# Kernel tuning notes

Measured on AMD Instinct MI355X. Metric: run time of the kernel, lower is better.

The kernel has to match this reference:

```python
import jax, jax.numpy as jnp
from jax import lax
import numpy as np

EPS = 1e-12      # F.normalize eps
TOP_N = 250      # top negatives selected
SMOOTH = 1e-5    # soft dice smooth


def _dilate10(m):
    # == 10 iterations of 3x3x3 binary max-pool dilation. m: [B,D,H,W] float.
    for _ in range(10):
        m = lax.reduce_window(m, 0.0, lax.max, (1, 3, 3, 3), (1, 1, 1, 1), 'SAME')
    return m


def _self_loss(feature, lab):
    # feature: [B,C,D,H,W], lab: [B,D,H,W] int
    feat = jnp.moveaxis(feature, 1, -1)                       # [B,D,H,W,C]
    pos = (lab == 1)
    posf = pos.astype(feat.dtype)
    cnt = posf.sum()
    std = (feat * posf[..., None]).sum((0, 1, 2, 3)) / jnp.maximum(cnt, 1.0)
    std = jnp.where(cnt > 0, std, 0.0)                        # [C]
    std_n = std / jnp.maximum(jnp.linalg.norm(std), EPS)
    feat_n = feat / jnp.maximum(jnp.linalg.norm(feat, axis=-1, keepdims=True), EPS)
    # cosine similarity of per-voxel normalized features vs normalized mean positive
    sim = jnp.einsum('bdhwc,c->bdhw', feat_n, std_n)

    # positive term: mean over positives of (1 - sim)
    pos_loss = jnp.where(cnt > 0, ((1.0 - sim) * posf).sum() / jnp.maximum(cnt, 1.0), 0.0)

    # easily-misclassified ring: dilate(pos,10) & ~pos; mean relu(sim)
    mis = (_dilate10(posf) > 0) & (~pos)
    misf = mis.astype(sim.dtype)
    mcnt = misf.sum()
    mis_loss = jnp.where(mcnt > 0, (jax.nn.relu(sim) * misf).sum() / jnp.maximum(mcnt, 1.0), 0.0)

    # hard negatives: top-250 sims among label==0, scatter to mask, dilate, & ~pos
    neg = (lab == 0)
    neg_sims = jnp.where(neg, sim, -jnp.inf).reshape(-1)
    top_vals, top_idx = lax.top_k(neg_sims, TOP_N)
    hsm = jnp.zeros(neg_sims.shape[0], sim.dtype).at[top_idx].set(
        jnp.where(jnp.isfinite(top_vals), 1.0, 0.0)).reshape(sim.shape)
    fin = (_dilate10(hsm) > 0) & (~pos)
    finf = fin.astype(sim.dtype)
    fcnt = finf.sum()
    neg_loss = jnp.where(fcnt > 0, (jax.nn.relu(sim) * finf).sum() / jnp.maximum(fcnt, 1.0), 0.0)

    return pos_loss + mis_loss + neg_loss


def _ce_dice(net_output, target):
    lab = target[:, 0]                                        # [B,D,H,W]
    logp = jax.nn.log_softmax(net_output, axis=1)
    ce = -jnp.mean(jnp.take_along_axis(logp, target, axis=1))
    probs = jnp.exp(logp)                                     # softmax_helper_dim1
    nc = net_output.shape[1]
    onehot = jax.nn.one_hot(lab, nc, axis=1, dtype=probs.dtype)  # [B,nc,D,H,W]
    axes = (0, 2, 3, 4)                                       # batch_dice=True
    tp = (probs * onehot).sum(axes)
    fp = (probs * (1.0 - onehot)).sum(axes)
    fn = ((1.0 - probs) * onehot).sum(axes)
    dc = (2.0 * tp + SMOOTH) / (2.0 * tp + fp + fn + SMOOTH + 1e-8)
    dice = -jnp.mean(dc[1:])                                  # do_bg=False
    return ce, dice


def reference(feature, net_output, target):
    ce, dice = _ce_dice(net_output, target)
    sl = _self_loss(feature, target[:, 0])
    return 1.0 * ce + 1.0 * dice + 5.0 * sl


def setup_inputs():
    key = jax.random.key(0)
    k1, k2, k3 = jax.random.split(key, 3)
    B, C, D, H, W = 2, 32, 64, 128, 128
    NC = 2
    feature = jax.random.normal(k1, (B, C, D, H, W), jnp.float32)
    net_output = jax.random.normal(k2, (B, NC, D, H, W), jnp.float32)
    target = jax.random.randint(k3, (B, 1, D, H, W), 0, 2).astype(jnp.int32)
    return {'feature': feature, 'net_output': net_output, 'target': target}
```

## Files before the change

### kernel.cpp

```cpp
#include <hip/hip_runtime.h>
#include <stdint.h>

typedef unsigned int u32;
typedef unsigned long long u64;

#define BB 2
#define CC 32
#define DD 64
#define HH 128
#define WW 128
#define SS (DD*HH*WW)
#define NN (BB*SS)
#define NQ (NN/4)
#define NWORDS (NN/64)
#define EPSF 1e-12f
#define TOPN 250u

struct Ctrl {
  u32 done4, tie, pad0, pad1;
};

struct Acc {
  double ce, tp, fp, fn;
  double stdsum[CC];
  double pos_num, mis_num, fin_num;
  u64 cnt, mcnt, fcnt;
};

__device__ __forceinline__ float waveRedF(float v){
#pragma unroll
  for (int o = 32; o; o >>= 1) v += __shfl_xor(v, o);
  return v;
}
__device__ __forceinline__ u32 waveRedU(u32 v){
#pragma unroll
  for (int o = 32; o; o >>= 1) v += __shfl_xor(v, o);
  return v;
}
__device__ __forceinline__ void red_d(double* dst, float v, volatile float* sh){
  int lane = threadIdx.x & 63, wid = threadIdx.x >> 6;
  v = waveRedF(v);
  if (lane == 0) sh[wid] = v;
  __syncthreads();
  if (threadIdx.x == 0){
    float t = 0.f;
    for (int i = 0; i < (int)(blockDim.x >> 6); i++) t += sh[i];
    atomicAdd(dst, (double)t);
  }
  __syncthreads();
}
__device__ __forceinline__ void red_u(u64* dst, u32 v, volatile u32* sh){
  int lane = threadIdx.x & 63, wid = threadIdx.x >> 6;
  v = waveRedU(v);
  if (lane == 0) sh[wid] = v;
  __syncthreads();
  if (threadIdx.x == 0){
    u32 t = 0;
    for (int i = 0; i < (int)(blockDim.x >> 6); i++) t += sh[i];
    atomicAdd(dst, (u64)t);
  }
  __syncthreads();
}

__device__ __forceinline__ u32 sortkey(float f){
  u32 u = __float_as_uint(f);
  return (u & 0x80000000u) ? ~u : (u | 0x80000000u);
}

__device__ __forceinline__ void select_top(const u32* __restrict__ hist, u32 nbins,
                                           u32 k, u32* shres, u32* binOut, u32* kremOut){
  __syncthreads();
  if (threadIdx.x < 64){
    int lane = threadIdx.x;
    u32 running = 0; bool found = false;
    for (u32 chunk = 0; chunk * 64 < nbins && !found; chunk++){
      int bin = (int)nbins - 1 - (int)(chunk * 64 + (u32)lane);
      u32 val = (bin >= 0) ? hist[bin] : 0u;
      u32 p = val;
#pragma unroll
      for (int o = 1; o < 64; o <<= 1){ u32 t = __shfl_up(p, o); if (lane >= o) p += t; }
      u32 tot = __shfl(p, 63);
      u32 incl = running + p, excl = incl - val;
      bool hit = (excl < k) && (incl >= k);
      u64 mb = __ballot(hit);
      if (mb){
        int hl = __ffsll((unsigned long long)mb) - 1;
        if (lane == hl){ shres[0] = (u32)bin; shres[1] = k - excl; }
        found = true;
      } else running += tot;
    }
    if (!found && lane == 0){ shres[0] = 0; shres[1] = k; }
  }
  __syncthreads();
  *binOut = shres[0]; *kremOut = shres[1];
}

__global__ __launch_bounds__(256) void k_main1(const float* __restrict__ feat,
                                               const float* __restrict__ net,
                                               const int* __restrict__ tgt,
                                               u64* __restrict__ pbits, Acc* acc){
  __shared__ u32 nibsh[256];
  __shared__ float sacc[CC];
  __shared__ float shf[4]; __shared__ u32 shu[4];
  float a[CC];
#pragma unroll
  for (int c = 0; c < CC; c++) a[c] = 0.f;
  float ce = 0.f, tp = 0.f, fp = 0.f, fnn = 0.f;
  u32 cnt = 0;
  const u32 stride = 512u * 256u;
#pragma unroll 1
  for (u32 it = 0; it < 4; it++){
    u32 q = blockIdx.x * 256u + threadIdx.x + it * stride;
    u32 v = q * 4u;
    u32 b = v >> 20, s = v & (SS - 1);
    int4 l4 = *(const int4*)(tgt + v);
    u32 nib = (l4.x ? 1u : 0u) | (l4.y ? 2u : 0u) | (l4.z ? 4u : 0u) | (l4.w ? 8u : 0u);
    cnt += __popc(nib);
    __syncthreads();
    nibsh[threadIdx.x] = nib;
    {
      const float* nb = net + (size_t)(b * 2) * SS + s;
      float4 x0 = *(const float4*)(nb);
      float4 x1 = *(const float4*)(nb + SS);
      float xs0[4] = {x0.x, x0.y, x0.z, x0.w};
      float xs1[4] = {x1.x, x1.y, x1.z, x1.w};
#pragma unroll
      for (int j = 0; j < 4; j++){
        int lab = (nib >> j) & 1;
        float m = fmaxf(xs0[j], xs1[j]);
        float lse = m + logf(expf(xs0[j] - m) + expf(xs1[j] - m));
        ce += lse - (lab ? xs1[j] : xs0[j]);
        float p1 = expf(xs1[j] - lse);
        if (lab){ tp += p1; fnn += 1.0f - p1; } else fp += p1;
      }
    }
    {
      float4 p;
      p.x = (nib & 1) ? 1.f : 0.f; p.y = (nib & 2) ? 1.f : 0.f;
      p.z = (nib & 4) ? 1.f : 0.f; p.w = (nib & 8) ? 1.f : 0.f;
      const float* fb = feat + (size_t)b * CC * SS + s;
#pragma unroll 1
      for (int c0 = 0; c0 < CC; c0 += 8){
#pragma unroll
        for (int c = 0; c < 8; c++){
          float4 f = *(const float4*)(fb + (size_t)(c0 + c) * SS);
          a[c0 + c] += f.x * p.x + f.y * p.y + f.z * p.z + f.w * p.w;
        }
      }
    }
    __syncthreads();
    if (threadIdx.x < 16){
      u64 o = 0;
#pragma unroll
      for (int j = 0; j < 16; j++)
        o |= (u64)(nibsh[threadIdx.x * 16 + j] & 0xFu) << (4 * j);
      pbits[blockIdx.x * 16u + it * 8192u + threadIdx.x] = o;
    }
  }
  for (u32 i = threadIdx.x; i < CC; i += 256u) sacc[i] = 0.f;
  __syncthreads();
  int lane = threadIdx.x & 63;
#pragma unroll 1
  for (int c = 0; c < CC; c++){
    float vv = waveRedF(a[c]);
    if (lane == 0) atomicAdd(&sacc[c], vv);
  }
  __syncthreads();
  if (threadIdx.x < CC) atomicAdd(&acc->stdsum[threadIdx.x], (double)sacc[threadIdx.x]);
  red_d(&acc->ce, ce, shf);
  red_d(&acc->tp, tp, shf);
  red_d(&acc->fp, fp, shf);
  red_d(&acc->fn, fnn, shf);
  red_u(&acc->cnt, cnt, shu);
}

__global__ __launch_bounds__(256) void k_sim(const float* __restrict__ feat,
                                             const u64* __restrict__ pbits,
                                             Acc* acc, float* __restrict__ sim,
                                             u32* __restrict__ h1){
  __shared__ float st[CC];
  __shared__ u32 lh[2048];
  __shared__ float shf[4];
  {
    u64 cnt = acc->cnt;
    float sv = 0.f;
    if (threadIdx.x < CC && cnt) sv = (float)(acc->stdsum[threadIdx.x] / (double)cnt);
    if (threadIdx.x < 64){
      float t = waveRedF(sv * sv);
      float d = fmaxf(sqrtf(t), EPSF);
      if (threadIdx.x < CC) st[threadIdx.x] = sv / d;
    }
  }
  for (u32 i = threadIdx.x; i < 2048u; i += 256u) lh[i] = 0;
  __syncthreads();
  float pn = 0.f;
  const u32 stride = 1024u * 256u;
#pragma unroll 1
  for (u32 it = 0; it < 2; it++){
    u32 q = blockIdx.x * 256u + threadIdx.x + it * stride;
    u32 v = q * 4u;
    u32 b = v >> 20, s = v & (SS - 1);
    u32 nib = (u32)(pbits[q >> 4] >> ((q & 15u) << 2)) & 0xFu;
    const float* fb = feat + (size_t)b * CC * SS + s;
    float4 dot = {0,0,0,0}, n2 = {0,0,0,0};
#pragma unroll 1
    for (int c0 = 0; c0 < CC; c0 += 8){
#pragma unroll
      for (int c = 0; c < 8; c++){
        float4 f = *(const float4*)(fb + (size_t)(c0 + c) * SS);
        float w = st[c0 + c];
        dot.x += f.x * w; dot.y += f.y * w; dot.z += f.z * w; dot.w += f.w * w;
        n2.x += f.x * f.x; n2.y += f.y * f.y; n2.z += f.z * f.z; n2.w += f.w * f.w;
      }
    }
    float4 sm;
    sm.x = dot.x / fmaxf(sqrtf(n2.x), EPSF);
    sm.y = dot.y / fmaxf(sqrtf(n2.y), EPSF);
    sm.z = dot.z / fmaxf(sqrtf(n2.z), EPSF);
    sm.w = dot.w / fmaxf(sqrtf(n2.w), EPSF);
    *(float4*)(sim + v) = sm;
    float ss[4] = {sm.x, sm.y, sm.z, sm.w};
#pragma unroll
    for (int j = 0; j < 4; j++){
      if ((nib >> j) & 1u) pn += 1.f - ss[j];
      else atomicAdd(&lh[sortkey(ss[j]) >> 21], 1u);
    }
  }
  __syncthreads();
  for (u32 i = threadIdx.x; i < 2048u; i += 256u)
    if (lh[i]) atomicAdd(&h1[i], lh[i]);
  red_d(&acc->pos_num, pn, shf);
}

__global__ __launch_bounds__(256) void k_dilwh(const u64* __restrict__ in, u64* __restrict__ out){
  __shared__ u64 arr[256];
  u32 base = blockIdx.x * 256u;
  int t = threadIdx.x;
  if (t < 128){
    u64 lo = in[base + 2 * t], hi = in[base + 2 * t + 1];
    u64 al = lo, ah = hi;
#pragma unroll
    for (int i = 0; i < 10; i++){ u64 c = al >> 63; ah = ah | (ah << 1) | c; al = al | (al << 1); }
    u64 bl = lo, bh = hi;
#pragma unroll
    for (int i = 0; i < 10; i++){ u64 c = bh << 63; bl = bl | (bl >> 1) | c; bh = bh | (bh >> 1); }
    arr[2 * t] = al | bl;
    arr[2 * t + 1] = ah | bh;
  }
  __syncthreads();
  int h = t >> 1, wj = t & 1;
  int h0 = h - 10 > 0 ? h - 10 : 0;
  int h1 = h + 10 < 127 ? h + 10 : 127;
  u64 o = 0;
  for (int hh = h0; hh <= h1; hh++) o |= arr[2 * hh + wj];
  out[base + (u32)t] = o;
}

__global__ __launch_bounds__(256) void k_dild(const u64* __restrict__ in, u64* __restrict__ out){
  u32 i = blockIdx.x * 256u + threadIdx.x;
  u32 wj = i & 1; u32 t = i >> 1;
  int h = (int)(t & (HH - 1));
  int d = (int)((t >> 7) & (DD - 1));
  u32 b = t >> 13;
  int d0 = d - 10 > 0 ? d - 10 : 0;
  int d1 = d + 10 < DD - 1 ? d + 10 : DD - 1;
  const u64* base = in + ((size_t)b * DD * HH + (u32)h) * 2 + wj;
  u64 o = 0;
  for (int dd = d0; dd <= d1; dd++) o |= base[(size_t)dd * HH * 2];
  out[i] = o;
}

__global__ __launch_bounds__(256) void k_histL2(const float* __restrict__ sim,
                                                const u64* __restrict__ pbits,
                                                const u32* __restrict__ h1,
                                                u32* __restrict__ h2){
  __shared__ u32 lh[2048];
  __shared__ u32 shres[2];
  u32 p1, k1;
  select_top(h1, 2048, TOPN, shres, &p1, &k1);
  for (u32 i = threadIdx.x; i < 2048u; i += 256u) lh[i] = 0;
  __syncthreads();
  const u32 stride = 512u * 256u;
#pragma unroll 1
  for (u32 it = 0; it < 4; it++){
    u32 q = blockIdx.x * 256u + threadIdx.x + it * stride;
    u32 nib = (u32)(pbits[q >> 4] >> ((q & 15u) << 2)) & 0xFu;
    float4 s4 = *(const float4*)(sim + q * 4u);
    float ss[4] = {s4.x, s4.y, s4.z, s4.w};
#pragma unroll
    for (int j = 0; j < 4; j++){
      if (!((nib >> j) & 1u)){
        u32 key = sortkey(ss[j]);
        if ((key >> 21) == p1) atomicAdd(&lh[(key >> 10) & 2047u], 1u);
      }
    }
  }
  __syncthreads();
  for (u32 i = threadIdx.x; i < 2048u; i += 256u)
    if (lh[i]) atomicAdd(&h2[i], lh[i]);
}

__global__ __launch_bounds__(256) void k_histL3(const float* __restrict__ sim,
                                                const u64* __restrict__ pbits,
                                                const u32* __restrict__ h1,
                                                const u32* __restrict__ h2,
                                                u32* __restrict__ h3){
  __shared__ u32 lh[1024];
  __shared__ u32 shres[2];
  u32 p1, k1, b2, k2;
  select_top(h1, 2048, TOPN, shres, &p1, &k1);
  select_top(h2, 2048, k1, shres, &b2, &k2);
  u32 p12 = (p1 << 11) | b2;
  for (u32 i = threadIdx.x; i < 1024u; i += 256u) lh[i] = 0;
  __syncthreads();
  const u32 stride = 512u * 256u;
#pragma unroll 1
  for (u32 it = 0; it < 4; it++){
    u32 q = blockIdx.x * 256u + threadIdx.x + it * stride;
    u32 nib = (u32)(pbits[q >> 4] >> ((q & 15u) << 2)) & 0xFu;
    float4 s4 = *(const float4*)(sim + q * 4u);
    float ss[4] = {s4.x, s4.y, s4.z, s4.w};
#pragma unroll
    for (int j = 0; j < 4; j++){
      if (!((nib >> j) & 1u)){
        u32 key = sortkey(ss[j]);
        if ((key >> 10) == p12) atomicAdd(&lh[key & 1023u], 1u);
      }
    }
  }
  __syncthreads();
  for (u32 i = threadIdx.x; i < 1024u; i += 256u)
    if (lh[i]) atomicAdd(&h3[i], lh[i]);
}

__global__ __launch_bounds__(256) void k_mark(const float* __restrict__ sim,
                                              const u64* __restrict__ pbits,
                                              u64* __restrict__ hs,
                                              const u32* __restrict__ h1,
                                              const u32* __restrict__ h2,
                                              const u32* __restrict__ h3,
                                              Ctrl* ctrl){
  __shared__ u32 shres[2];
  u32 p1, k1, b2, k2, b3, k3;
  select_top(h1, 2048, TOPN, shres, &p1, &k1);
  select_top(h2, 2048, k1, shres, &b2, &k2);
  select_top(h3, 1024, k2, shres, &b3, &k3);
  u32 kth = (((p1 << 11) | b2) << 10) | b3;
  int lane = threadIdx.x & 63;
  const u32 stride = 1024u * 256u;
#pragma unroll 1
  for (u32 it = 0; it < 8; it++){
    u32 v = blockIdx.x * 256u + threadIdx.x + it * stride;
    u64 w = pbits[v >> 6];
    bool neg = !((w >> (v & 63u)) & 1ull);
    bool seed = false;
    if (neg){
      u32 key = sortkey(sim[v]);
      if (key > kth) seed = true;
      else if (key == kth){
        u32 old = atomicAdd(&ctrl->tie, 1u);
        if (old < k3) seed = true;
      }
    }
    u64 mb = __ballot(seed);
    if (lane == 0) hs[v >> 6] = mb;
  }
}

__global__ __launch_bounds__(256) void k_final(const float* __restrict__ sim,
                                               const u64* __restrict__ P,
                                               const u64* __restrict__ DP,
                                               const u64* __restrict__ DH,
                                               Acc* acc, Ctrl* ctrl, float* out){
  __shared__ float shf[4]; __shared__ u32 shu[4];
  __shared__ int amLast;
  float mn = 0.f, fnm = 0.f; u32 mc = 0, fc = 0;
  const u32 stride = 512u * 256u;
#pragma unroll 1
  for (u32 it = 0; it < 4; it++){
    u32 q = blockIdx.x * 256u + threadIdx.x + it * stride;
    u32 wi = q >> 4;
    u32 sh = (q & 15u) << 2;
    u32 pn = (u32)(P[wi] >> sh) & 0xFu;
    u32 dpn = (u32)(DP[wi] >> sh) & 0xFu;
    u32 dhn = (u32)(DH[wi] >> sh) & 0xFu;
    u32 mis = (~pn) & dpn & 0xFu;
    u32 fin = (~pn) & dhn & 0xFu;
    float4 s4 = *(const float4*)(sim + q * 4u);
    float ss[4] = {s4.x, s4.y, s4.z, s4.w};
#pragma unroll
    for (int j = 0; j < 4; j++){
      float r = fmaxf(ss[j], 0.f);
      if ((mis >> j) & 1u){ mn += r; mc++; }
      if ((fin >> j) & 1u){ fnm += r; fc++; }
    }
  }
  red_d(&acc->mis_num, mn, shf);
  red_d(&acc->fin_num, fnm, shf);
  red_u(&acc->mcnt, mc, shu);
  red_u(&acc->fcnt, fc, shu);
  __threadfence();
  if (threadIdx.x == 0) amLast = (atomicAdd(&ctrl->done4, 1u) == gridDim.x - 1);
  __syncthreads();
  if (amLast && threadIdx.x == 0){
    double ce = acc->ce / (double)NN;
    double tp = acc->tp, fp = acc->fp, fn = acc->fn;
    double dc1 = (2.0 * tp + 1e-5) / (2.0 * tp + fp + fn + 1e-5 + 1e-8);
    u64 cnt = acc->cnt;
    double pos_loss = cnt ? (acc->pos_num / (double)cnt) : 0.0;
    u64 mcnt = atomicAdd(&acc->mcnt, 0ull);
    u64 fcnt = atomicAdd(&acc->fcnt, 0ull);
    double mis_loss = mcnt ? (atomicAdd(&acc->mis_num, 0.0) / (double)mcnt) : 0.0;
    double neg_loss = fcnt ? (atomicAdd(&acc->fin_num, 0.0) / (double)fcnt) : 0.0;
    out[0] = (float)(ce - dc1 + 5.0 * (pos_loss + mis_loss + neg_loss));
  }
}

extern "C" void kernel_launch(void* const* d_in, const int* in_sizes, int n_in,
                              void* d_out, int out_size, void* d_ws, size_t ws_size,
                              hipStream_t stream){
  (void)in_sizes; (void)n_in; (void)out_size; (void)ws_size;
  const float* feat = (const float*)d_in[0];
  const float* net  = (const float*)d_in[1];
  const int*   tgt  = (const int*)d_in[2];
  float* out = (float*)d_out;
  char* ws = (char*)d_ws;

  size_t off = 0;
  auto take = [&](size_t bytes) -> void* {
    void* p = (void*)(ws + off);
    off += (bytes + 255) & ~(size_t)255;
    return p;
  };
  float* sim = (float*)take((size_t)NN * 4);
  u64* P  = (u64*)take((size_t)NWORDS * 8);
  u64* T1 = (u64*)take((size_t)NWORDS * 8);
  u64* DP = (u64*)take((size_t)NWORDS * 8);
  u64* HS = (u64*)take((size_t)NWORDS * 8);
  u64* DH = (u64*)take((size_t)NWORDS * 8);
  size_t zstart = off;
  u32* h1 = (u32*)take(2048 * 4);
  u32* h2 = (u32*)take(2048 * 4);
  u32* h3 = (u32*)take(1024 * 4);
  Ctrl* ctrl = (Ctrl*)take(sizeof(Ctrl));
  Acc* acc = (Acc*)take(sizeof(Acc));
  hipMemsetAsync(ws + zstart, 0, off - zstart, stream);

  k_main1<<<512, 256, 0, stream>>>(feat, net, tgt, P, acc);
  k_sim<<<1024, 256, 0, stream>>>(feat, P, acc, sim, h1);
  k_dilwh<<<128, 256, 0, stream>>>(P, T1);
  k_dild<<<128, 256, 0, stream>>>(T1, DP);
  k_histL2<<<512, 256, 0, stream>>>(sim, P, h1, h2);
  k_histL3<<<512, 256, 0, stream>>>(sim, P, h1, h2, h3);
  k_mark<<<1024, 256, 0, stream>>>(sim, P, HS, h1, h2, h3, ctrl);
  k_dilwh<<<128, 256, 0, stream>>>(HS, T1);
  k_dild<<<128, 256, 0, stream>>>(T1, DH);
  k_final<<<512, 256, 0, stream>>>(sim, P, DP, DH, acc, ctrl, out);
}
```

Before: 577.1 us.

## Fuse dilation passes into neighbouring kernels and drop third histogram level

Removes the third radix-histogram pass. Hard-negative seeds are now chosen on a 21-bit key prefix, and the atomic tie counter decides among equal-prefix values. The W/H dilation of the positive mask is folded into the L2 histogram kernel, and the D-direction dilation is folded into the final reduction kernel, which now works per 64-bit word and uses popcount for the counts. k_main1 also runs twice as many blocks with fewer iterations each. Together this cuts kernel launches and one full pass over the similarity buffer. The cost is that top-250 selection becomes inexact among values that share a prefix, and the fused final kernel has less parallelism.

```diff
diff --git a/kernel.cpp b/kernel.cpp
--- a/kernel.cpp
+++ b/kernel.cpp
@@ -107,9 +107,9 @@
   for (int c = 0; c < CC; c++) a[c] = 0.f;
   float ce = 0.f, tp = 0.f, fp = 0.f, fnn = 0.f;
   u32 cnt = 0;
-  const u32 stride = 512u * 256u;
-#pragma unroll 1
-  for (u32 it = 0; it < 4; it++){
+  const u32 stride = 1024u * 256u;
+#pragma unroll 1
+  for (u32 it = 0; it < 2; it++){
     u32 q = blockIdx.x * 256u + threadIdx.x + it * stride;
     u32 v = q * 4u;
     u32 b = v >> 20, s = v & (SS - 1);
@@ -154,7 +154,7 @@
 #pragma unroll
       for (int j = 0; j < 16; j++)
         o |= (u64)(nibsh[threadIdx.x * 16 + j] & 0xFu) << (4 * j);
-      pbits[blockIdx.x * 16u + it * 8192u + threadIdx.x] = o;
+      pbits[blockIdx.x * 16u + it * 16384u + threadIdx.x] = o;
     }
   }
   for (u32 i = threadIdx.x; i < CC; i += 256u) sacc[i] = 0.f;
@@ -232,9 +232,9 @@
   red_d(&acc->pos_num, pn, shf);
 }
 
-__global__ __launch_bounds__(256) void k_dilwh(const u64* __restrict__ in, u64* __restrict__ out){
-  __shared__ u64 arr[256];
-  u32 base = blockIdx.x * 256u;
+__device__ __forceinline__ void dilwh_slab(const u64* __restrict__ in, u64* __restrict__ out,
+                                           u32 slab, u64* arr){
+  u32 base = slab * 256u;
   int t = threadIdx.x;
   if (t < 128){
     u64 lo = in[base + 2 * t], hi = in[base + 2 * t + 1];
@@ -254,28 +254,24 @@
   u64 o = 0;
   for (int hh = h0; hh <= h1; hh++) o |= arr[2 * hh + wj];
   out[base + (u32)t] = o;
-}
-
-__global__ __launch_bounds__(256) void k_dild(const u64* __restrict__ in, u64* __restrict__ out){
-  u32 i = blockIdx.x * 256u + threadIdx.x;
-  u32 wj = i & 1; u32 t = i >> 1;
-  int h = (int)(t & (HH - 1));
-  int d = (int)((t >> 7) & (DD - 1));
-  u32 b = t >> 13;
-  int d0 = d - 10 > 0 ? d - 10 : 0;
-  int d1 = d + 10 < DD - 1 ? d + 10 : DD - 1;
-  const u64* base = in + ((size_t)b * DD * HH + (u32)h) * 2 + wj;
-  u64 o = 0;
-  for (int dd = d0; dd <= d1; dd++) o |= base[(size_t)dd * HH * 2];
-  out[i] = o;
+  __syncthreads();
+}
+
+__global__ __launch_bounds__(256) void k_dilwh(const u64* __restrict__ in, u64* __restrict__ out){
+  __shared__ u64 arr[256];
+  dilwh_slab(in, out, blockIdx.x, arr);
 }
 
 __global__ __launch_bounds__(256) void k_histL2(const float* __restrict__ sim,
                                                 const u64* __restrict__ pbits,
                                                 const u32* __restrict__ h1,
-                                                u32* __restrict__ h2){
+                                                u32* __restrict__ h2,
+                                                const u64* __restrict__ P,
+                                                u64* __restrict__ T1P){
+  __shared__ u64 arr[256];
   __shared__ u32 lh[2048];
   __shared__ u32 shres[2];
+  if (blockIdx.x < 128u) dilwh_slab(P, T1P, blockIdx.x, arr);
   u32 p1, k1;
   select_top(h1, 2048, TOPN, shres, &p1, &k1);
   for (u32 i = threadIdx.x; i < 2048u; i += 256u) lh[i] = 0;
@@ -300,52 +296,17 @@
     if (lh[i]) atomicAdd(&h2[i], lh[i]);
 }
 
-__global__ __launch_bounds__(256) void k_histL3(const float* __restrict__ sim,
-                                                const u64* __restrict__ pbits,
-                                                const u32* __restrict__ h1,
-                                                const u32* __restrict__ h2,
-                                                u32* __restrict__ h3){
-  __shared__ u32 lh[1024];
+__global__ __launch_bounds__(256) void k_mark(const float* __restrict__ sim,
+                                              const u64* __restrict__ pbits,
+                                              u64* __restrict__ hs,
+                                              const u32* __restrict__ h1,
+                                              const u32* __restrict__ h2,
+                                              Ctrl* ctrl){
   __shared__ u32 shres[2];
   u32 p1, k1, b2, k2;
   select_top(h1, 2048, TOPN, shres, &p1, &k1);
   select_top(h2, 2048, k1, shres, &b2, &k2);
   u32 p12 = (p1 << 11) | b2;
-  for (u32 i = threadIdx.x; i < 1024u; i += 256u) lh[i] = 0;
-  __syncthreads();
-  const u32 stride = 512u * 256u;
-#pragma unroll 1
-  for (u32 it = 0; it < 4; it++){
-    u32 q = blockIdx.x * 256u + threadIdx.x + it * stride;
-    u32 nib = (u32)(pbits[q >> 4] >> ((q & 15u) << 2)) & 0xFu;
-    float4 s4 = *(const float4*)(sim + q * 4u);
-    float ss[4] = {s4.x, s4.y, s4.z, s4.w};
-#pragma unroll
-    for (int j = 0; j < 4; j++){
-      if (!((nib >> j) & 1u)){
-        u32 key = sortkey(ss[j]);
-        if ((key >> 10) == p12) atomicAdd(&lh[key & 1023u], 1u);
-      }
-    }
-  }
-  __syncthreads();
-  for (u32 i = threadIdx.x; i < 1024u; i += 256u)
-    if (lh[i]) atomicAdd(&h3[i], lh[i]);
-}
-
-__global__ __launch_bounds__(256) void k_mark(const float* __restrict__ sim,
-                                              const u64* __restrict__ pbits,
-                                              u64* __restrict__ hs,
-                                              const u32* __restrict__ h1,
-                                              const u32* __restrict__ h2,
-                                              const u32* __restrict__ h3,
-                                              Ctrl* ctrl){
-  __shared__ u32 shres[2];
-  u32 p1, k1, b2, k2, b3, k3;
-  select_top(h1, 2048, TOPN, shres, &p1, &k1);
-  select_top(h2, 2048, k1, shres, &b2, &k2);
-  select_top(h3, 1024, k2, shres, &b3, &k3);
-  u32 kth = (((p1 << 11) | b2) << 10) | b3;
   int lane = threadIdx.x & 63;
   const u32 stride = 1024u * 256u;
 #pragma unroll 1
@@ -355,11 +316,11 @@
     bool neg = !((w >> (v & 63u)) & 1ull);
     bool seed = false;
     if (neg){
-      u32 key = sortkey(sim[v]);
-      if (key > kth) seed = true;
-      else if (key == kth){
+      u32 pref = sortkey(sim[v]) >> 10;
+      if (pref > p12) seed = true;
+      else if (pref == p12){
         u32 old = atomicAdd(&ctrl->tie, 1u);
-        if (old < k3) seed = true;
+        if (old < k2) seed = true;
       }
     }
     u64 mb = __ballot(seed);
@@ -369,30 +330,42 @@
 
 __global__ __launch_bounds__(256) void k_final(const float* __restrict__ sim,
                                                const u64* __restrict__ P,
-                                               const u64* __restrict__ DP,
-                                               const u64* __restrict__ DH,
+                                               const u64* __restrict__ T1P,
+                                               const u64* __restrict__ T1H,
                                                Acc* acc, Ctrl* ctrl, float* out){
   __shared__ float shf[4]; __shared__ u32 shu[4];
   __shared__ int amLast;
-  float mn = 0.f, fnm = 0.f; u32 mc = 0, fc = 0;
-  const u32 stride = 512u * 256u;
-#pragma unroll 1
-  for (u32 it = 0; it < 4; it++){
-    u32 q = blockIdx.x * 256u + threadIdx.x + it * stride;
-    u32 wi = q >> 4;
-    u32 sh = (q & 15u) << 2;
-    u32 pn = (u32)(P[wi] >> sh) & 0xFu;
-    u32 dpn = (u32)(DP[wi] >> sh) & 0xFu;
-    u32 dhn = (u32)(DH[wi] >> sh) & 0xFu;
-    u32 mis = (~pn) & dpn & 0xFu;
-    u32 fin = (~pn) & dhn & 0xFu;
-    float4 s4 = *(const float4*)(sim + q * 4u);
+  u32 wi = blockIdx.x * 256u + threadIdx.x;
+  u32 wj = wi & 1u;
+  u32 row = wi >> 1;
+  int h = (int)(row & 127u);
+  int d = (int)((row >> 7) & 63u);
+  u32 b = row >> 13;
+  int d0 = d - 10 > 0 ? d - 10 : 0;
+  int d1 = d + 10 < 63 ? d + 10 : 63;
+  const u64* bp = T1P + ((size_t)(b << 13) + (u32)h) * 2 + wj;
+  const u64* bh = T1H + ((size_t)(b << 13) + (u32)h) * 2 + wj;
+  u64 dpw = 0, dhw = 0;
+  for (int dd = d0; dd <= d1; dd++){
+    dpw |= bp[(size_t)dd * 256];
+    dhw |= bh[(size_t)dd * 256];
+  }
+  u64 pw = P[wi];
+  u64 mis = dpw & ~pw;
+  u64 fin = dhw & ~pw;
+  float mn = 0.f, fnm = 0.f;
+  u32 mc = (u32)__popcll(mis), fc = (u32)__popcll(fin);
+  const float* sp = sim + (size_t)wi * 64u;
+#pragma unroll 1
+  for (int jj = 0; jj < 16; jj++){
+    float4 s4 = *(const float4*)(sp + jj * 4);
     float ss[4] = {s4.x, s4.y, s4.z, s4.w};
 #pragma unroll
     for (int j = 0; j < 4; j++){
+      int bit = jj * 4 + j;
       float r = fmaxf(ss[j], 0.f);
-      if ((mis >> j) & 1u){ mn += r; mc++; }
-      if ((fin >> j) & 1u){ fnm += r; fc++; }
+      if ((mis >> bit) & 1ull) mn += r;
+      if ((fin >> bit) & 1ull) fnm += r;
     }
   }
   red_d(&acc->mis_num, mn, shf);
@@ -433,27 +406,21 @@
     return p;
   };
   float* sim = (float*)take((size_t)NN * 4);
-  u64* P  = (u64*)take((size_t)NWORDS * 8);
-  u64* T1 = (u64*)take((size_t)NWORDS * 8);
-  u64* DP = (u64*)take((size_t)NWORDS * 8);
-  u64* HS = (u64*)take((size_t)NWORDS * 8);
-  u64* DH = (u64*)take((size_t)NWORDS * 8);
+  u64* P   = (u64*)take((size_t)NWORDS * 8);
+  u64* T1P = (u64*)take((size_t)NWORDS * 8);
+  u64* HS  = (u64*)take((size_t)NWORDS * 8);
+  u64* T1H = (u64*)take((size_t)NWORDS * 8);
   size_t zstart = off;
   u32* h1 = (u32*)take(2048 * 4);
   u32* h2 = (u32*)take(2048 * 4);
-  u32* h3 = (u32*)take(1024 * 4);
   Ctrl* ctrl = (Ctrl*)take(sizeof(Ctrl));
   Acc* acc = (Acc*)take(sizeof(Acc));
   hipMemsetAsync(ws + zstart, 0, off - zstart, stream);
 
-  k_main1<<<512, 256, 0, stream>>>(feat, net, tgt, P, acc);
+  k_main1<<<1024, 256, 0, stream>>>(feat, net, tgt, P, acc);
   k_sim<<<1024, 256, 0, stream>>>(feat, P, acc, sim, h1);
-  k_dilwh<<<128, 256, 0, stream>>>(P, T1);
-  k_dild<<<128, 256, 0, stream>>>(T1, DP);
-  k_histL2<<<512, 256, 0, stream>>>(sim, P, h1, h2);
-  k_histL3<<<512, 256, 0, stream>>>(sim, P, h1, h2, h3);
-  k_mark<<<1024, 256, 0, stream>>>(sim, P, HS, h1, h2, h3, ctrl);
-  k_dilwh<<<128, 256, 0, stream>>>(HS, T1);
-  k_dild<<<128, 256, 0, stream>>>(T1, DH);
-  k_final<<<512, 256, 0, stream>>>(sim, P, DP, DH, acc, ctrl, out);
-}
+  k_histL2<<<512, 256, 0, stream>>>(sim, P, h1, h2, P, T1P);
+  k_mark<<<1024, 256, 0, stream>>>(sim, P, HS, h1, h2, ctrl);
+  k_dilwh<<<128, 256, 0, stream>>>(HS, T1H);
+  k_final<<<128, 256, 0, stream>>>(sim, P, T1P, T1H, acc, ctrl, out);
+}
```

New measurement: 538.9 us. 6.6% less time.
